# Kernel tuning notes

Hardware: AMD Instinct MI355X
Metric: run time of the kernel (lower is better)

The kernel has to match this reference:

```python
import jax, jax.numpy as jnp
import numpy as np

N_NODES, N_EDGES, N_GRAPHS, EMB_DIM, IMG_DIM, N_TYPES = 50000, 800000, 64, 128, 4096, 30


def gcn_conv(x, W, b, row, col, ew, dis, n):
    # PyG GCNConv: x @ W.T, symmetric-normalized weighted aggregation with self-loops, + bias
    xw = x @ W.T                                            # [N, D]
    norm = dis[row] * ew * dis[col]                          # [E]
    agg = jax.ops.segment_sum(norm[:, None] * xw[row], col, num_segments=n)
    agg = agg + (dis * dis)[:, None] * xw                    # self-loop (weight 1) term
    return agg + b


def setup_inputs() -> dict:
    key = jax.random.key(0)
    ks = jax.random.split(key, 20)
    inp = {
        "images": jax.random.normal(ks[0], (N_GRAPHS, IMG_DIM), jnp.float32),
        "node_types": jax.random.randint(ks[1], (N_NODES,), 0, N_TYPES),
        "edge_index": jax.random.randint(ks[2], (2, N_EDGES), 0, N_NODES),
        "edge_attr": jax.random.uniform(ks[3], (N_EDGES,), jnp.float32),
        "batch": jnp.sort(jax.random.randint(ks[4], (N_NODES,), 0, N_GRAPHS)),
    }
    def lin(k, out_d, in_d):
        s = 1.0 / np.sqrt(in_d)
        kw, kb = jax.random.split(k)
        return (jax.random.uniform(kw, (out_d, in_d), jnp.float32, -s, s),
                jax.random.uniform(kb, (out_d,), jnp.float32, -s, s))
    inp["emb_table"] = jax.random.normal(ks[5], (N_TYPES, EMB_DIM), jnp.float32)
    inp["W_img"], inp["b_img"] = lin(ks[6], IMG_DIM, IMG_DIM)      # frozen image backbone head
    inp["W1"], inp["b1"] = lin(ks[7], EMB_DIM, EMB_DIM)
    inp["W2"], inp["b2"] = lin(ks[8], EMB_DIM, EMB_DIM)
    inp["W3"], inp["b3"] = lin(ks[9], EMB_DIM, EMB_DIM)
    inp["Wi"], inp["bi"] = lin(ks[10], EMB_DIM, IMG_DIM)
    inp["Wc"], inp["bc"] = lin(ks[11], EMB_DIM, IMG_DIM + EMB_DIM)
    return inp


def reference(images, node_types, edge_index, edge_attr, batch, emb_table,
              W_img, b_img, W1, b1, W2, b2, W3, b3, Wi, bi, Wc, bc):
    n = node_types.shape[0]
    B = images.shape[0]
    row, col = edge_index[0], edge_index[1]
    # gcn_norm with self-loops (fill value 1): deg at aggregation endpoint (col)
    deg = jax.ops.segment_sum(edge_attr, col, num_segments=n) + 1.0
    dis = jax.lax.rsqrt(deg)
    # frozen image model (linear stand-in for VGG fc head, output dim 4096)
    xi = images @ W_img.T + b_img                           # [B, 4096]
    # encode_images branch
    oi = xi @ Wi.T + bi
    oi = oi / jnp.linalg.norm(oi, axis=1, keepdims=True)
    # encode_images_with_graphs branch
    xg = emb_table[node_types]                              # [N, D]
    xg = jax.nn.relu(gcn_conv(xg, W1, b1, row, col, edge_attr, dis, n))
    xg = jax.nn.relu(gcn_conv(xg, W2, b2, row, col, edge_attr, dis, n))
    xg = gcn_conv(xg, W3, b3, row, col, edge_attr, dis, n)
    cnt = jax.ops.segment_sum(jnp.ones((n,), xg.dtype), batch, num_segments=B)
    pooled = jax.ops.segment_sum(xg, batch, num_segments=B) / jnp.maximum(cnt, 1.0)[:, None]
    oc = jnp.concatenate([xi, pooled], axis=1) @ Wc.T + bc
    oc = oc / jnp.linalg.norm(oc, axis=1, keepdims=True)
    return (oi, oc)
```

## Files before the change

### kernel.cpp

```cpp
#include <hip/hip_runtime.h>
#include <math.h>

#define NN 50000
#define NE 800000
#define NG 64
#define D 128
#define IMG 4096
#define NT 30
#define CAP 64

#define EBLK (NE / 256)
#define PBLK ((NT * D + 2 * D * 64) / 256)
#define CBLK (64 * IMG / 2 / 256)
#define GBLK ((NN + 63) / 64)
#define IMGBLK ((IMG / 64) * 8)
#define IREDBLK (64 * IMG / 256)

typedef unsigned int uint;
typedef unsigned short ushort;
typedef __attribute__((ext_vector_type(8))) __bf16 bf16x8;
typedef __attribute__((ext_vector_type(4))) float f32x4;

__device__ __forceinline__ uint bf16rne(float f) {
  uint h = __float_as_uint(f);
  return (h + 0x7fffu + ((h >> 16) & 1u)) >> 16;
}
__device__ __forceinline__ uint pack2bf(float a, float b) {
  return bf16rne(a) | (bf16rne(b) << 16);
}
__device__ __forceinline__ float bflo(uint u) { return __uint_as_float(u << 16); }
__device__ __forceinline__ float bfhi(uint u) { return __uint_as_float(u & 0xffff0000u); }



__global__ __launch_bounds__(256) void setup_multi(
    const int* __restrict__ row, const int* __restrict__ col,
    const float* __restrict__ ew, int* __restrict__ cnt, int2* __restrict__ ebuf,
    const float* __restrict__ emb, const float* __restrict__ W1, float* __restrict__ embW,
    const float* __restrict__ W2, const float* __restrict__ W3,
    uint* __restrict__ Wbf2, uint* __restrict__ Wbf3,
    const float* __restrict__ images, uint* __restrict__ imgAbf,
    const int* __restrict__ batch, int* __restrict__ goff) {
  int b = blockIdx.x;
  if (b < EBLK) {
    int e = b * 256 + threadIdx.x;
    if (e < NE) {
      int c = col[e];
      int s = atomicAdd(&cnt[c], 1);
      if (s < CAP) ebuf[((size_t)c << 6) + s] = make_int2(row[e], __float_as_int(ew[e]));
    }
  } else if (b < EBLK + PBLK) {
    int tid = (b - EBLK) * 256 + threadIdx.x;
    if (tid < NT * D) {
      int tt = tid >> 7, nn2 = tid & 127;
      const float* ep = emb + (size_t)tt * D;
      const float* wp = W1 + (size_t)nn2 * D;
      float acc = 0.f;
      for (int k = 0; k < D; k += 4) {
        float4 evv = *(const float4*)(ep + k);
        float4 wvv = *(const float4*)(wp + k);
        acc += evv.x * wvv.x + evv.y * wvv.y + evv.z * wvv.z + evv.w * wvv.w;
      }
      embW[tid] = acc;
    } else if (tid < NT * D + D * 64) {
      int j = tid - NT * D;
      float2 v = ((const float2*)W2)[j];
      Wbf2[j] = pack2bf(v.x, v.y);
    } else {
      int j = tid - NT * D - D * 64;
      float2 v = ((const float2*)W3)[j];
      Wbf3[j] = pack2bf(v.x, v.y);
    }
  } else if (b < EBLK + PBLK + CBLK) {
    int idx = (b - EBLK - PBLK) * 256 + threadIdx.x;
    float2 v = ((const float2*)images)[idx];
    imgAbf[idx] = pack2bf(v.x, v.y);
  } else {
    int g = threadIdx.x;
    if (g <= NG) {
      int lo = 0, hi = NN;
      while (lo < hi) {
        int mid = (lo + hi) >> 1;
        if (batch[mid] < g) lo = mid + 1; else hi = mid;
      }
      goff[g] = lo;
    }
  }
}


__global__ __launch_bounds__(256) void node_dis(const int* __restrict__ cnt,
                                                const int2* __restrict__ ebuf,
                                                float* __restrict__ dis) {
  int lane = threadIdx.x & 63;
  int sub = lane >> 4, fl = lane & 15;
  int node = (blockIdx.x * 4 + (threadIdx.x >> 6)) * 4 + sub;
  if (node >= NN) return;
  int n = min(cnt[node], CAP);
  const int2* eb = ebuf + ((size_t)node << 6);
  float acc = 0.f;
  for (int j = fl; j < n; j += 16) acc += __int_as_float(eb[j].y);
  acc += __shfl_xor(acc, 8);
  acc += __shfl_xor(acc, 4);
  acc += __shfl_xor(acc, 2);
  acc += __shfl_xor(acc, 1);
  if (fl == 0) dis[node] = 1.0f / sqrtf(acc + 1.0f);
}


__global__ __launch_bounds__(256) void lay1_fused(const int* __restrict__ cnt,
                                                  const int2* __restrict__ ebuf,
                                                  const float* __restrict__ dis,
                                                  const int* __restrict__ types,
                                                  const float* __restrict__ embW,
                                                  const float* __restrict__ b1,
                                                  uint* __restrict__ outbf) {
  __shared__ float sE[NT * D];
  __shared__ float sB[D];
  int t = threadIdx.x;
  for (int i = t; i < NT * D; i += 256) sE[i] = embW[i];
  if (t < D) sB[t] = b1[t];
  __syncthreads();
  int wave = t >> 6, lane = t & 63;
  #pragma unroll
  for (int r = 0; r < 4; r++) {
    int node = blockIdx.x * 16 + wave * 4 + r;
    if (node >= NN) continue;
    float ax = sB[2 * lane], ay = sB[2 * lane + 1];
    int n = min(cnt[node], CAP);
    const int2* eb = ebuf + ((size_t)node << 6);
    float disc = dis[node];
    int idx = 0;
    for (; idx + 4 <= n; idx += 4) {
      int4 ra = *(const int4*)(eb + idx);
      int4 rb = *(const int4*)(eb + idx + 2);
      float n0 = dis[ra.x] * __int_as_float(ra.y) * disc;
      float n1 = dis[ra.z] * __int_as_float(ra.w) * disc;
      float n2 = dis[rb.x] * __int_as_float(rb.y) * disc;
      float n3 = dis[rb.z] * __int_as_float(rb.w) * disc;
      float2 e0 = *(const float2*)&sE[types[ra.x] * D + 2 * lane];
      float2 e1 = *(const float2*)&sE[types[ra.z] * D + 2 * lane];
      float2 e2 = *(const float2*)&sE[types[rb.x] * D + 2 * lane];
      float2 e3 = *(const float2*)&sE[types[rb.z] * D + 2 * lane];
      ax = fmaf(n0, e0.x, ax); ay = fmaf(n0, e0.y, ay);
      ax = fmaf(n1, e1.x, ax); ay = fmaf(n1, e1.y, ay);
      ax = fmaf(n2, e2.x, ax); ay = fmaf(n2, e2.y, ay);
      ax = fmaf(n3, e3.x, ax); ay = fmaf(n3, e3.y, ay);
    }
    for (; idx < n; idx++) {
      int2 rr = eb[idx];
      float nm = dis[rr.x] * __int_as_float(rr.y) * disc;
      float2 ev = *(const float2*)&sE[types[rr.x] * D + 2 * lane];
      ax = fmaf(nm, ev.x, ax);
      ay = fmaf(nm, ev.y, ay);
    }
    float dd = disc * disc;
    float2 es = *(const float2*)&sE[types[node] * D + 2 * lane];
    ax = fmaf(dd, es.x, ax);
    ay = fmaf(dd, es.y, ay);
    ax = fmaxf(ax, 0.f);
    ay = fmaxf(ay, 0.f);
    outbf[(size_t)node * 64 + lane] = pack2bf(ax, ay);
  }
}


__device__ __forceinline__ void node_gemm_body(const uint* __restrict__ Abf,
                                               const uint* __restrict__ Wbf,
                                               uint* __restrict__ outbf, int bx,
                                               ushort* __restrict__ tile) {
  int w = threadIdx.x >> 6, lane = threadIdx.x & 63;
  int quad = lane >> 4;
  int m0 = bx * 64 + w * 16;
  int mrow = m0 + (lane & 15);
  int arow = (mrow < NN) ? mrow : 0;
  uint4 afr[4];
  #pragma unroll
  for (int ks = 0; ks < 4; ks++)
    afr[ks] = *(const uint4*)(Abf + (size_t)arow * 64 + ks * 16 + quad * 4);
  f32x4 acc[8] = {};
  #pragma unroll
  for (int nt = 0; nt < 8; nt++) {
    int n = nt * 16 + (lane & 15);
    #pragma unroll
    for (int ks = 0; ks < 4; ks++) {
      union { uint4 u; bf16x8 v; } au, bu;
      au.u = afr[ks];
      bu.u = *(const uint4*)(Wbf + (size_t)n * 64 + ks * 16 + quad * 4);
      acc[nt] = __builtin_amdgcn_mfma_f32_16x16x32_bf16(au.v, bu.v, acc[nt], 0, 0, 0);
    }
  }
  ushort* tw = tile + w * 16 * 136;
  #pragma unroll
  for (int nt = 0; nt < 8; nt++)
    #pragma unroll
    for (int i = 0; i < 4; i++)
      tw[(quad * 4 + i) * 136 + nt * 16 + (lane & 15)] = (ushort)bf16rne(acc[nt][i]);
  __builtin_amdgcn_s_waitcnt(0);
  #pragma unroll
  for (int rep = 0; rep < 4; rep++) {
    int r = rep * 4 + quad;
    int j = lane & 15;
    int node = m0 + r;
    if (node < NN) {
      uint4 v = *(const uint4*)&tw[r * 136 + j * 8];
      *(uint4*)(outbf + (size_t)node * 64 + j * 4) = v;
    }
  }
}


__device__ __forceinline__ void img_mfma_body(const uint* __restrict__ Abf,
                                              const float* __restrict__ W,
                                              float* __restrict__ splitbuf, int bx, int by) {
  int wv = threadIdx.x >> 6, lane = threadIdx.x & 63;
  int n = bx * 64 + wv * 16 + (lane & 15);
  int kq = (lane >> 4) * 8;
  int k0 = by * 512 + kq;
  f32x4 acc[4] = {{0.f, 0.f, 0.f, 0.f}, {0.f, 0.f, 0.f, 0.f},
                  {0.f, 0.f, 0.f, 0.f}, {0.f, 0.f, 0.f, 0.f}};
  const float* wp = W + (size_t)n * IMG + k0;
  const uint* ap = Abf + (size_t)(lane & 15) * (IMG / 2) + k0 / 2;
  for (int ks = 0; ks < 512; ks += 32) {
    float4 w0 = *(const float4*)(wp + ks);
    float4 w1 = *(const float4*)(wp + ks + 4);
    union { uint4 u; bf16x8 v; } bu;
    bu.u.x = pack2bf(w0.x, w0.y);
    bu.u.y = pack2bf(w0.z, w0.w);
    bu.u.z = pack2bf(w1.x, w1.y);
    bu.u.w = pack2bf(w1.z, w1.w);
    #pragma unroll
    for (int mt = 0; mt < 4; mt++) {
      union { uint4 u; bf16x8 v; } au;
      au.u = *(const uint4*)(ap + (size_t)mt * 16 * (IMG / 2) + ks / 2);
      acc[mt] = __builtin_amdgcn_mfma_f32_16x16x32_bf16(au.v, bu.v, acc[mt], 0, 0, 0);
    }
  }
  #pragma unroll
  for (int mt = 0; mt < 4; mt++)
    #pragma unroll
    for (int i = 0; i < 4; i++) {
      int m = mt * 16 + (lane >> 4) * 4 + i;
      splitbuf[((size_t)by * 64 + m) * IMG + n] = acc[mt][i];
    }
}

__global__ __launch_bounds__(256) void gemm2_plus_img(const uint* __restrict__ bufX,
                                                      const uint* __restrict__ wbf2,
                                                      uint* __restrict__ bufB,
                                                      const uint* __restrict__ imgAbf,
                                                      const float* __restrict__ Wimg,
                                                      float* __restrict__ splitbuf) {
  __shared__ ushort tile[4 * 16 * 136];
  int b = blockIdx.x;
  if (b < GBLK) {
    node_gemm_body(bufX, wbf2, bufB, b, tile);
  } else {
    int j = b - GBLK;
    img_mfma_body(imgAbf, Wimg, splitbuf, j & 63, j >> 6);
  }
}

__global__ __launch_bounds__(256) void gemm3_plus_imgred(const uint* __restrict__ bufX,
                                                         const uint* __restrict__ wbf3,
                                                         uint* __restrict__ bufB,
                                                         const float* __restrict__ splitbuf,
                                                         const float* __restrict__ b_img,
                                                         float* __restrict__ xcat) {
  __shared__ ushort tile[4 * 16 * 136];
  int b = blockIdx.x;
  if (b < GBLK) {
    node_gemm_body(bufX, wbf3, bufB, b, tile);
  } else {
    int idx = (b - GBLK) * 256 + threadIdx.x;
    if (idx < 64 * IMG) {
      float acc = b_img[idx & (IMG - 1)];
      #pragma unroll
      for (int s = 0; s < 8; s++) acc += splitbuf[(size_t)s * 64 * IMG + idx];
      xcat[(size_t)(idx >> 12) * (IMG + D) + (idx & (IMG - 1))] = acc;
    }
  }
}


__global__ __launch_bounds__(256) void aggregate2(const uint* __restrict__ xw,
                                                  const int* __restrict__ cnt,
                                                  const int2* __restrict__ ebuf,
                                                  const float* __restrict__ dis,
                                                  const float* __restrict__ bias, int relu,
                                                  uint* __restrict__ outbf) {
  const uint2* xw2 = (const uint2*)xw;
  int wave = threadIdx.x >> 6;
  int lane = threadIdx.x & 63;
  int half = lane >> 5;
  int fl = lane & 31;
  int node = (blockIdx.x * 4 + wave) * 2 + half;
  if (node >= NN) return;
  float a0 = 0.f, a1 = 0.f, a2 = 0.f, a3 = 0.f;
  int n = min(cnt[node], CAP);
  const int2* eb = ebuf + ((size_t)node << 6);
  float disc = dis[node];
  int idx = 0;
  for (; idx + 8 <= n; idx += 8) {
    int4 ra = *(const int4*)(eb + idx);
    int4 rb = *(const int4*)(eb + idx + 2);
    int4 rc = *(const int4*)(eb + idx + 4);
    int4 rd = *(const int4*)(eb + idx + 6);
    float n0 = dis[ra.x] * __int_as_float(ra.y) * disc;
    float n1 = dis[ra.z] * __int_as_float(ra.w) * disc;
    float n2 = dis[rb.x] * __int_as_float(rb.y) * disc;
    float n3 = dis[rb.z] * __int_as_float(rb.w) * disc;
    float n4 = dis[rc.x] * __int_as_float(rc.y) * disc;
    float n5 = dis[rc.z] * __int_as_float(rc.w) * disc;
    float n6 = dis[rd.x] * __int_as_float(rd.y) * disc;
    float n7 = dis[rd.z] * __int_as_float(rd.w) * disc;
    uint2 u0 = xw2[(size_t)ra.x * 32 + fl];
    uint2 u1 = xw2[(size_t)ra.z * 32 + fl];
    uint2 u2 = xw2[(size_t)rb.x * 32 + fl];
    uint2 u3 = xw2[(size_t)rb.z * 32 + fl];
    uint2 u4 = xw2[(size_t)rc.x * 32 + fl];
    uint2 u5 = xw2[(size_t)rc.z * 32 + fl];
    uint2 u6 = xw2[(size_t)rd.x * 32 + fl];
    uint2 u7 = xw2[(size_t)rd.z * 32 + fl];
    a0 = fmaf(n0, bflo(u0.x), a0); a1 = fmaf(n0, bfhi(u0.x), a1);
    a2 = fmaf(n0, bflo(u0.y), a2); a3 = fmaf(n0, bfhi(u0.y), a3);
    a0 = fmaf(n1, bflo(u1.x), a0); a1 = fmaf(n1, bfhi(u1.x), a1);
    a2 = fmaf(n1, bflo(u1.y), a2); a3 = fmaf(n1, bfhi(u1.y), a3);
    a0 = fmaf(n2, bflo(u2.x), a0); a1 = fmaf(n2, bfhi(u2.x), a1);
    a2 = fmaf(n2, bflo(u2.y), a2); a3 = fmaf(n2, bfhi(u2.y), a3);
    a0 = fmaf(n3, bflo(u3.x), a0); a1 = fmaf(n3, bfhi(u3.x), a1);
    a2 = fmaf(n3, bflo(u3.y), a2); a3 = fmaf(n3, bfhi(u3.y), a3);
    a0 = fmaf(n4, bflo(u4.x), a0); a1 = fmaf(n4, bfhi(u4.x), a1);
    a2 = fmaf(n4, bflo(u4.y), a2); a3 = fmaf(n4, bfhi(u4.y), a3);
    a0 = fmaf(n5, bflo(u5.x), a0); a1 = fmaf(n5, bfhi(u5.x), a1);
    a2 = fmaf(n5, bflo(u5.y), a2); a3 = fmaf(n5, bfhi(u5.y), a3);
    a0 = fmaf(n6, bflo(u6.x), a0); a1 = fmaf(n6, bfhi(u6.x), a1);
    a2 = fmaf(n6, bflo(u6.y), a2); a3 = fmaf(n6, bfhi(u6.y), a3);
    a0 = fmaf(n7, bflo(u7.x), a0); a1 = fmaf(n7, bfhi(u7.x), a1);
    a2 = fmaf(n7, bflo(u7.y), a2); a3 = fmaf(n7, bfhi(u7.y), a3);
  }
  for (; idx + 2 <= n; idx += 2) {
    int4 ra = *(const int4*)(eb + idx);
    float n0 = dis[ra.x] * __int_as_float(ra.y) * disc;
    float n1 = dis[ra.z] * __int_as_float(ra.w) * disc;
    uint2 u0 = xw2[(size_t)ra.x * 32 + fl];
    uint2 u1 = xw2[(size_t)ra.z * 32 + fl];
    a0 = fmaf(n0, bflo(u0.x), a0); a1 = fmaf(n0, bfhi(u0.x), a1);
    a2 = fmaf(n0, bflo(u0.y), a2); a3 = fmaf(n0, bfhi(u0.y), a3);
    a0 = fmaf(n1, bflo(u1.x), a0); a1 = fmaf(n1, bfhi(u1.x), a1);
    a2 = fmaf(n1, bflo(u1.y), a2); a3 = fmaf(n1, bfhi(u1.y), a3);
  }
  if (idx < n) {
    int2 r = eb[idx];
    float nm = dis[r.x] * __int_as_float(r.y) * disc;
    uint2 u = xw2[(size_t)r.x * 32 + fl];
    a0 = fmaf(nm, bflo(u.x), a0);
    a1 = fmaf(nm, bfhi(u.x), a1);
    a2 = fmaf(nm, bflo(u.y), a2);
    a3 = fmaf(nm, bfhi(u.y), a3);
  }
  float dd = disc * disc;
  {
    uint2 u = xw2[(size_t)node * 32 + fl];
    a0 = fmaf(dd, bflo(u.x), a0);
    a1 = fmaf(dd, bfhi(u.x), a1);
    a2 = fmaf(dd, bflo(u.y), a2);
    a3 = fmaf(dd, bfhi(u.y), a3);
  }
  float4 b = *(const float4*)(bias + 4 * fl);
  a0 += b.x; a1 += b.y; a2 += b.z; a3 += b.w;
  if (relu) {
    a0 = fmaxf(a0, 0.f);
    a1 = fmaxf(a1, 0.f);
    a2 = fmaxf(a2, 0.f);
    a3 = fmaxf(a3, 0.f);
  }
  uint2 o;
  o.x = pack2bf(a0, a1);
  o.y = pack2bf(a2, a3);
  ((uint2*)outbf)[(size_t)node * 32 + fl] = o;
}


__device__ __forceinline__ void gemm64_body(const float* __restrict__ A, int lda,
                                            const float* __restrict__ W,
                                            const float* __restrict__ bias,
                                            float* __restrict__ out, int N, int K,
                                            int kChunk, int bx, int by,
                                            float (*xs)[68], float (*ws)[68]) {
  int t = threadIdx.x;
  int n0 = bx * 64;
  int k0 = by * kChunk;
  int kEnd = min(K, k0 + kChunk);
  int tn = t & 15;
  int tm = t >> 4;
  float acc[4][4] = {};
  if (by == 0) {
    #pragma unroll
    for (int ni = 0; ni < 4; ni++) {
      float bv = bias[n0 + tn * 4 + ni];
      #pragma unroll
      for (int mi = 0; mi < 4; mi++) acc[mi][ni] = bv;
    }
  }
  for (int kt = k0; kt < kEnd; kt += 16) {
    int kc = (t & 3) * 4;
    int rr = t >> 2;
    float4 va = *(const float4*)(A + (size_t)rr * lda + kt + kc);
    xs[kc + 0][rr] = va.x; xs[kc + 1][rr] = va.y; xs[kc + 2][rr] = va.z; xs[kc + 3][rr] = va.w;
    float4 vw = *(const float4*)(W + (size_t)(n0 + rr) * K + kt + kc);
    ws[kc + 0][rr] = vw.x; ws[kc + 1][rr] = vw.y; ws[kc + 2][rr] = vw.z; ws[kc + 3][rr] = vw.w;
    __syncthreads();
    #pragma unroll
    for (int k = 0; k < 16; k++) {
      float4 xv = *(const float4*)&xs[k][tm * 4];
      float4 wv = *(const float4*)&ws[k][tn * 4];
      float xm[4] = {xv.x, xv.y, xv.z, xv.w};
      float wn[4] = {wv.x, wv.y, wv.z, wv.w};
      #pragma unroll
      for (int mi = 0; mi < 4; mi++)
        #pragma unroll
        for (int ni = 0; ni < 4; ni++)
          acc[mi][ni] = fmaf(xm[mi], wn[ni], acc[mi][ni]);
    }
    __syncthreads();
  }
  #pragma unroll
  for (int mi = 0; mi < 4; mi++)
    #pragma unroll
    for (int ni = 0; ni < 4; ni++)
      atomicAdd(&out[(size_t)(tm * 4 + mi) * N + n0 + tn * 4 + ni], acc[mi][ni]);
}


__global__ __launch_bounds__(256) void pool_gemm_oi(const uint* __restrict__ xb,
                                                    const int* __restrict__ goff,
                                                    float* __restrict__ xcat,
                                                    const float* __restrict__ Wi,
                                                    const float* __restrict__ bi,
                                                    float* __restrict__ oi_raw) {
  __shared__ float xs[16][68];
  __shared__ float ws[16][68];
  int b = blockIdx.x;
  if (b < 2 * NG) {
    int g = b >> 1;
    int chunk = ((b & 1) << 2) + (threadIdx.x >> 6);
    int fl = threadIdx.x & 63;
    int s = goff[g], e = goff[g + 1];
    float inv = 1.0f / fmaxf((float)(e - s), 1.0f);
    float ax = 0.f, ay = 0.f;
    for (int i = s + chunk; i < e; i += 8) {
      uint u = xb[(size_t)i * 64 + fl];
      ax += bflo(u);
      ay += bfhi(u);
    }
    atomicAdd(&xcat[(size_t)g * (IMG + D) + IMG + 2 * fl], ax * inv);
    atomicAdd(&xcat[(size_t)g * (IMG + D) + IMG + 2 * fl + 1], ay * inv);
  } else {
    int j = b - 2 * NG;
    gemm64_body(xcat, IMG + D, Wi, bi, oi_raw, D, IMG, 128, j & 1, j >> 1, xs, ws);
  }
}

__global__ __launch_bounds__(256) void gemm_oc(const float* __restrict__ xcat,
                                               const float* __restrict__ Wc,
                                               const float* __restrict__ bc,
                                               float* __restrict__ oc_raw) {
  __shared__ float xs[16][68];
  __shared__ float ws[16][68];
  int b = blockIdx.x;
  gemm64_body(xcat, IMG + D, Wc, bc, oc_raw, D, IMG + D, 176, b & 1, b >> 1, xs, ws);
}

__global__ __launch_bounds__(128) void normalize_rows(const float* __restrict__ oi_raw,
                                                      const float* __restrict__ oc_raw,
                                                      float* __restrict__ out) {
  int r = blockIdx.x;
  int t = threadIdx.x;
  const float* src = (r < 64) ? (oi_raw + r * D) : (oc_raw + (r - 64) * D);
  float v = src[t];
  __shared__ float red[128];
  red[t] = v * v;
  __syncthreads();
  for (int s = 64; s > 0; s >>= 1) {
    if (t < s) red[t] += red[t + s];
    __syncthreads();
  }
  out[r * D + t] = v / sqrtf(red[0]);
}


extern "C" void kernel_launch(void* const* d_in, const int* in_sizes, int n_in,
                              void* d_out, int out_size, void* d_ws, size_t ws_size,
                              hipStream_t stream) {
  const float* images = (const float*)d_in[0];
  const int* node_types = (const int*)d_in[1];
  const int* erow = (const int*)d_in[2];
  const int* ecol = erow + NE;
  const float* eattr = (const float*)d_in[3];
  const int* batch = (const int*)d_in[4];
  const float* emb = (const float*)d_in[5];
  const float* W_img = (const float*)d_in[6];
  const float* b_img = (const float*)d_in[7];
  const float* W1 = (const float*)d_in[8];
  const float* b1 = (const float*)d_in[9];
  const float* W2 = (const float*)d_in[10];
  const float* b2 = (const float*)d_in[11];
  const float* W3 = (const float*)d_in[12];
  const float* b3 = (const float*)d_in[13];
  const float* Wi = (const float*)d_in[14];
  const float* bi = (const float*)d_in[15];
  const float* Wc = (const float*)d_in[16];
  const float* bc = (const float*)d_in[17];
  float* out = (float*)d_out;

  char* w = (char*)d_ws;
  auto alloc = [&](size_t bytes) -> void* {
    void* p = (void*)w;
    w += (bytes + 511) & ~(size_t)511;
    return p;
  };
  int* cnt = (int*)alloc((size_t)NN * 4);
  float* xcat = (float*)alloc((size_t)64 * (IMG + D) * 4);
  float* oi_raw = (float*)alloc(64 * D * 4);
  float* oc_raw = (float*)alloc(64 * D * 4);
  size_t zero_bytes = (size_t)(w - (char*)d_ws);
  int* goff = (int*)alloc((NG + 1) * 4);
  float* dis = (float*)alloc(NN * 4);
  float* embW1 = (float*)alloc(NT * D * 4);
  uint* wbf2 = (uint*)alloc(D * 64 * 4);
  uint* wbf3 = (uint*)alloc(D * 64 * 4);
  int2* ebuf = (int2*)alloc((size_t)NN * CAP * 8);
  uint* bufX = (uint*)alloc((size_t)NN * D * 2);
  uint* bufB = (uint*)alloc((size_t)NN * D * 2);
  uint* imgAbf = (uint*)alloc((size_t)64 * IMG * 2);
  float* splitbuf = (float*)alloc((size_t)8 * 64 * IMG * 4);

  hipMemsetAsync(d_ws, 0, zero_bytes, stream);

  setup_multi<<<EBLK + PBLK + CBLK + 1, 256, 0, stream>>>(
      erow, ecol, eattr, cnt, ebuf, emb, W1, embW1, W2, W3, wbf2, wbf3,
      images, imgAbf, batch, goff);
  node_dis<<<(NN + 15) / 16, 256, 0, stream>>>(cnt, ebuf, dis);
  lay1_fused<<<(NN + 15) / 16, 256, 0, stream>>>(cnt, ebuf, dis, node_types, embW1, b1, bufX);
  gemm2_plus_img<<<GBLK + IMGBLK, 256, 0, stream>>>(bufX, wbf2, bufB, imgAbf, W_img, splitbuf);
  aggregate2<<<(NN + 7) / 8, 256, 0, stream>>>(bufB, cnt, ebuf, dis, b2, 1, bufX);
  gemm3_plus_imgred<<<GBLK + IREDBLK, 256, 0, stream>>>(bufX, wbf3, bufB, splitbuf, b_img, xcat);
  aggregate2<<<(NN + 7) / 8, 256, 0, stream>>>(bufB, cnt, ebuf, dis, b3, 0, bufX);
  pool_gemm_oi<<<2 * NG + 64, 256, 0, stream>>>(bufX, goff, xcat, Wi, bi, oi_raw);
  gemm_oc<<<48, 256, 0, stream>>>(xcat, Wc, bc, oc_raw);
  normalize_rows<<<128, 128, 0, stream>>>(oi_raw, oc_raw, out);
}
```

Measured before the change: 414.2 us.

## Split image GEMM across two launches, co-scheduled with node GEMM and aggregation

The image-head GEMM's K dimension is now split 16 ways instead of 8. Half of its blocks run alongside the layer-2 node GEMM and the other half alongside the layer-2 aggregation, so the large weight read is spread over two launches and overlaps the memory-bound graph work. The inner MFMA loop is restructured so each lane loads 16 contiguous weights per step. lay1_fused now uses 512-thread blocks. In exchange, splitbuf doubles in size and the reduction reads twice as many partial sums.

```diff
diff --git a/kernel.cpp b/kernel.cpp
--- a/kernel.cpp
+++ b/kernel.cpp
@@ -13,7 +13,9 @@
 #define PBLK ((NT * D + 2 * D * 64) / 256)
 #define CBLK (64 * IMG / 2 / 256)
 #define GBLK ((NN + 63) / 64)
-#define IMGBLK ((IMG / 64) * 8)
+#define AGGBLK ((NN + 7) / 8)
+#define KSPLIT 16
+#define IMGHALF (64 * KSPLIT / 2)
 #define IREDBLK (64 * IMG / 256)
 
 typedef unsigned int uint;
@@ -108,7 +110,7 @@
 }
 
 
-__global__ __launch_bounds__(256) void lay1_fused(const int* __restrict__ cnt,
+__global__ __launch_bounds__(512) void lay1_fused(const int* __restrict__ cnt,
                                                   const int2* __restrict__ ebuf,
                                                   const float* __restrict__ dis,
                                                   const int* __restrict__ types,
@@ -118,13 +120,13 @@
   __shared__ float sE[NT * D];
   __shared__ float sB[D];
   int t = threadIdx.x;
-  for (int i = t; i < NT * D; i += 256) sE[i] = embW[i];
+  for (int i = t; i < NT * D; i += 512) sE[i] = embW[i];
   if (t < D) sB[t] = b1[t];
   __syncthreads();
   int wave = t >> 6, lane = t & 63;
   #pragma unroll
   for (int r = 0; r < 4; r++) {
-    int node = blockIdx.x * 16 + wave * 4 + r;
+    int node = blockIdx.x * 32 + wave * 4 + r;
     if (node >= NN) continue;
     float ax = sB[2 * lane], ay = sB[2 * lane + 1];
     int n = min(cnt[node], CAP);
@@ -214,87 +216,60 @@
                                               const float* __restrict__ W,
                                               float* __restrict__ splitbuf, int bx, int by) {
   int wv = threadIdx.x >> 6, lane = threadIdx.x & 63;
+  int quad = lane >> 4;
   int n = bx * 64 + wv * 16 + (lane & 15);
-  int kq = (lane >> 4) * 8;
-  int k0 = by * 512 + kq;
+  int k0 = by * 256;
   f32x4 acc[4] = {{0.f, 0.f, 0.f, 0.f}, {0.f, 0.f, 0.f, 0.f},
                   {0.f, 0.f, 0.f, 0.f}, {0.f, 0.f, 0.f, 0.f}};
-  const float* wp = W + (size_t)n * IMG + k0;
-  const uint* ap = Abf + (size_t)(lane & 15) * (IMG / 2) + k0 / 2;
-  for (int ks = 0; ks < 512; ks += 32) {
-    float4 w0 = *(const float4*)(wp + ks);
-    float4 w1 = *(const float4*)(wp + ks + 4);
-    union { uint4 u; bf16x8 v; } bu;
-    bu.u.x = pack2bf(w0.x, w0.y);
-    bu.u.y = pack2bf(w0.z, w0.w);
-    bu.u.z = pack2bf(w1.x, w1.y);
-    bu.u.w = pack2bf(w1.z, w1.w);
+  const float* wp = W + (size_t)n * IMG + k0 + quad * 16;
+  const uint* ap = Abf + (size_t)(lane & 15) * (IMG / 2) + k0 / 2 + quad * 8;
+  #pragma unroll
+  for (int ss = 0; ss < 4; ss++) {
+    float4 w0 = *(const float4*)(wp + ss * 64);
+    float4 w1 = *(const float4*)(wp + ss * 64 + 4);
+    float4 w2 = *(const float4*)(wp + ss * 64 + 8);
+    float4 w3 = *(const float4*)(wp + ss * 64 + 12);
+    union { uint4 u; bf16x8 v; } b1u, b2u;
+    b1u.u.x = pack2bf(w0.x, w0.y);
+    b1u.u.y = pack2bf(w0.z, w0.w);
+    b1u.u.z = pack2bf(w1.x, w1.y);
+    b1u.u.w = pack2bf(w1.z, w1.w);
+    b2u.u.x = pack2bf(w2.x, w2.y);
+    b2u.u.y = pack2bf(w2.z, w2.w);
+    b2u.u.z = pack2bf(w3.x, w3.y);
+    b2u.u.w = pack2bf(w3.z, w3.w);
     #pragma unroll
     for (int mt = 0; mt < 4; mt++) {
-      union { uint4 u; bf16x8 v; } au;
-      au.u = *(const uint4*)(ap + (size_t)mt * 16 * (IMG / 2) + ks / 2);
-      acc[mt] = __builtin_amdgcn_mfma_f32_16x16x32_bf16(au.v, bu.v, acc[mt], 0, 0, 0);
+      const uint* app = ap + (size_t)mt * 16 * (IMG / 2) + ss * 32;
+      union { uint4 u; bf16x8 v; } a1u, a2u;
+      a1u.u = *(const uint4*)(app);
+      a2u.u = *(const uint4*)(app + 4);
+      acc[mt] = __builtin_amdgcn_mfma_f32_16x16x32_bf16(a1u.v, b1u.v, acc[mt], 0, 0, 0);
+      acc[mt] = __builtin_amdgcn_mfma_f32_16x16x32_bf16(a2u.v, b2u.v, acc[mt], 0, 0, 0);
     }
   }
   #pragma unroll
   for (int mt = 0; mt < 4; mt++)
     #pragma unroll
     for (int i = 0; i < 4; i++) {
-      int m = mt * 16 + (lane >> 4) * 4 + i;
+      int m = mt * 16 + quad * 4 + i;
       splitbuf[((size_t)by * 64 + m) * IMG + n] = acc[mt][i];
     }
 }
 
-__global__ __launch_bounds__(256) void gemm2_plus_img(const uint* __restrict__ bufX,
-                                                      const uint* __restrict__ wbf2,
-                                                      uint* __restrict__ bufB,
-                                                      const uint* __restrict__ imgAbf,
-                                                      const float* __restrict__ Wimg,
-                                                      float* __restrict__ splitbuf) {
-  __shared__ ushort tile[4 * 16 * 136];
-  int b = blockIdx.x;
-  if (b < GBLK) {
-    node_gemm_body(bufX, wbf2, bufB, b, tile);
-  } else {
-    int j = b - GBLK;
-    img_mfma_body(imgAbf, Wimg, splitbuf, j & 63, j >> 6);
-  }
-}
-
-__global__ __launch_bounds__(256) void gemm3_plus_imgred(const uint* __restrict__ bufX,
-                                                         const uint* __restrict__ wbf3,
-                                                         uint* __restrict__ bufB,
-                                                         const float* __restrict__ splitbuf,
-                                                         const float* __restrict__ b_img,
-                                                         float* __restrict__ xcat) {
-  __shared__ ushort tile[4 * 16 * 136];
-  int b = blockIdx.x;
-  if (b < GBLK) {
-    node_gemm_body(bufX, wbf3, bufB, b, tile);
-  } else {
-    int idx = (b - GBLK) * 256 + threadIdx.x;
-    if (idx < 64 * IMG) {
-      float acc = b_img[idx & (IMG - 1)];
-      #pragma unroll
-      for (int s = 0; s < 8; s++) acc += splitbuf[(size_t)s * 64 * IMG + idx];
-      xcat[(size_t)(idx >> 12) * (IMG + D) + (idx & (IMG - 1))] = acc;
-    }
-  }
-}
-
-
-__global__ __launch_bounds__(256) void aggregate2(const uint* __restrict__ xw,
-                                                  const int* __restrict__ cnt,
-                                                  const int2* __restrict__ ebuf,
-                                                  const float* __restrict__ dis,
-                                                  const float* __restrict__ bias, int relu,
-                                                  uint* __restrict__ outbf) {
+
+__device__ __forceinline__ void aggregate2_body(const uint* __restrict__ xw,
+                                                const int* __restrict__ cnt,
+                                                const int2* __restrict__ ebuf,
+                                                const float* __restrict__ dis,
+                                                const float* __restrict__ bias, int relu,
+                                                uint* __restrict__ outbf, int blk) {
   const uint2* xw2 = (const uint2*)xw;
   int wave = threadIdx.x >> 6;
   int lane = threadIdx.x & 63;
   int half = lane >> 5;
   int fl = lane & 31;
-  int node = (blockIdx.x * 4 + wave) * 2 + half;
+  int node = (blk * 4 + wave) * 2 + half;
   if (node >= NN) return;
   float a0 = 0.f, a1 = 0.f, a2 = 0.f, a3 = 0.f;
   int n = min(cnt[node], CAP);
@@ -381,6 +356,70 @@
   ((uint2*)outbf)[(size_t)node * 32 + fl] = o;
 }
 
+__global__ __launch_bounds__(256) void gemm2_plus_img(const uint* __restrict__ bufX,
+                                                      const uint* __restrict__ wbf2,
+                                                      uint* __restrict__ bufB,
+                                                      const uint* __restrict__ imgAbf,
+                                                      const float* __restrict__ Wimg,
+                                                      float* __restrict__ splitbuf) {
+  __shared__ ushort tile[4 * 16 * 136];
+  int b = blockIdx.x;
+  if (b < GBLK) {
+    node_gemm_body(bufX, wbf2, bufB, b, tile);
+  } else {
+    int j = b - GBLK;
+    img_mfma_body(imgAbf, Wimg, splitbuf, j & 63, j >> 6);
+  }
+}
+
+__global__ __launch_bounds__(256) void agg2_plus_img(const uint* __restrict__ bufB,
+                                                     const int* __restrict__ cnt,
+                                                     const int2* __restrict__ ebuf,
+                                                     const float* __restrict__ dis,
+                                                     const float* __restrict__ b2,
+                                                     uint* __restrict__ bufX,
+                                                     const uint* __restrict__ imgAbf,
+                                                     const float* __restrict__ Wimg,
+                                                     float* __restrict__ splitbuf) {
+  int b = blockIdx.x;
+  if (b < AGGBLK) {
+    aggregate2_body(bufB, cnt, ebuf, dis, b2, 1, bufX, b);
+  } else {
+    int j = b - AGGBLK;
+    img_mfma_body(imgAbf, Wimg, splitbuf, j & 63, 8 + (j >> 6));
+  }
+}
+
+__global__ __launch_bounds__(256) void gemm3_plus_imgred(const uint* __restrict__ bufX,
+                                                         const uint* __restrict__ wbf3,
+                                                         uint* __restrict__ bufB,
+                                                         const float* __restrict__ splitbuf,
+                                                         const float* __restrict__ b_img,
+                                                         float* __restrict__ xcat) {
+  __shared__ ushort tile[4 * 16 * 136];
+  int b = blockIdx.x;
+  if (b < GBLK) {
+    node_gemm_body(bufX, wbf3, bufB, b, tile);
+  } else {
+    int idx = (b - GBLK) * 256 + threadIdx.x;
+    if (idx < 64 * IMG) {
+      float acc = b_img[idx & (IMG - 1)];
+      #pragma unroll
+      for (int s = 0; s < KSPLIT; s++) acc += splitbuf[(size_t)s * 64 * IMG + idx];
+      xcat[(size_t)(idx >> 12) * (IMG + D) + (idx & (IMG - 1))] = acc;
+    }
+  }
+}
+
+__global__ __launch_bounds__(256) void aggregate2(const uint* __restrict__ xw,
+                                                  const int* __restrict__ cnt,
+                                                  const int2* __restrict__ ebuf,
+                                                  const float* __restrict__ dis,
+                                                  const float* __restrict__ bias, int relu,
+                                                  uint* __restrict__ outbf) {
+  aggregate2_body(xw, cnt, ebuf, dis, bias, relu, outbf, blockIdx.x);
+}
+
 
 __device__ __forceinline__ void gemm64_body(const float* __restrict__ A, int lda,
                                             const float* __restrict__ W,
@@ -534,7 +573,7 @@
   uint* bufX = (uint*)alloc((size_t)NN * D * 2);
   uint* bufB = (uint*)alloc((size_t)NN * D * 2);
   uint* imgAbf = (uint*)alloc((size_t)64 * IMG * 2);
-  float* splitbuf = (float*)alloc((size_t)8 * 64 * IMG * 4);
+  float* splitbuf = (float*)alloc((size_t)KSPLIT * 64 * IMG * 4);
 
   hipMemsetAsync(d_ws, 0, zero_bytes, stream);
 
@@ -542,11 +581,14 @@
       erow, ecol, eattr, cnt, ebuf, emb, W1, embW1, W2, W3, wbf2, wbf3,
       images, imgAbf, batch, goff);
   node_dis<<<(NN + 15) / 16, 256, 0, stream>>>(cnt, ebuf, dis);
-  lay1_fused<<<(NN + 15) / 16, 256, 0, stream>>>(cnt, ebuf, dis, node_types, embW1, b1, bufX);
-  gemm2_plus_img<<<GBLK + IMGBLK, 256, 0, stream>>>(bufX, wbf2, bufB, imgAbf, W_img, splitbuf);
-  aggregate2<<<(NN + 7) / 8, 256, 0, stream>>>(bufB, cnt, ebuf, dis, b2, 1, bufX);
-  gemm3_plus_imgred<<<GBLK + IREDBLK, 256, 0, stream>>>(bufX, wbf3, bufB, splitbuf, b_img, xcat);
-  aggregate2<<<(NN + 7) / 8, 256, 0, stream>>>(bufB, cnt, ebuf, dis, b3, 0, bufX);
+  lay1_fused<<<(NN + 31) / 32, 512, 0, stream>>>(cnt, ebuf, dis, node_types, embW1, b1, bufX);
+  gemm2_plus_img<<<GBLK + IMGHALF, 256, 0, stream>>>(bufX, wbf2, bufB, imgAbf, W_img,
+                                                     splitbuf);
+  agg2_plus_img<<<AGGBLK + IMGHALF, 256, 0, stream>>>(bufB, cnt, ebuf, dis, b2, bufX,
+                                                      imgAbf, W_img, splitbuf);
+  gemm3_plus_imgred<<<GBLK + IREDBLK, 256, 0, stream>>>(bufX, wbf3, bufB, splitbuf, b_img,
+                                                        xcat);
+  aggregate2<<<AGGBLK, 256, 0, stream>>>(bufB, cnt, ebuf, dis, b3, 0, bufX);
   pool_gemm_oi<<<2 * NG + 64, 256, 0, stream>>>(bufX, goff, xcat, Wi, bi, oi_raw);
   gemm_oc<<<48, 256, 0, stream>>>(xcat, Wc, bc, oc_raw);
   normalize_rows<<<128, 128, 0, stream>>>(oi_raw, oc_raw, out);
```

Measured after the change: 422.6 us. 1.02x slower.
